# Performance work log

Measured on AMD Instinct MI355X. Metric: run time of the kernel, lower is better.

## Reference

```python
import jax, jax.numpy as jnp
import numpy as np

EMBED_DIM = 2048
NUM_HEADS = 32
NUM_SEQS = 8
SEQ_LEN = 1024
TOTAL_TOKENS = NUM_SEQS * SEQ_LEN


def setup_inputs() -> dict:
    key = jax.random.key(0)
    ks = jax.random.split(key, 9)
    E = EMBED_DIM
    std = 0.02
    return {
        "hidden_states": jax.random.normal(ks[0], (TOTAL_TOKENS, E), dtype=jnp.float32),
        "Wq": jax.random.normal(ks[1], (E, E), dtype=jnp.float32) * std,
        "bq": jax.random.normal(ks[2], (E,), dtype=jnp.float32) * std,
        "Wk": jax.random.normal(ks[3], (E, E), dtype=jnp.float32) * std,
        "bk": jax.random.normal(ks[4], (E,), dtype=jnp.float32) * std,
        "Wv": jax.random.normal(ks[5], (E, E), dtype=jnp.float32) * std,
        "bv": jax.random.normal(ks[6], (E,), dtype=jnp.float32) * std,
        "Wo": jax.random.normal(ks[7], (E, E), dtype=jnp.float32) * std,
        "bo": jax.random.normal(ks[8], (E,), dtype=jnp.float32) * std,
        "seq_len": SEQ_LEN,
    }


def reference(hidden_states, Wq, bq, Wk, bk, Wv, bv, Wo, bo, seq_len):
    # OPTAttention (has_cache=False): block-diagonal causal attention over
    # packed ragged sequences; here all NUM_SEQS sequences have length seq_len,
    # so the block-diagonal mask is exactly per-sequence causal attention.
    T, E = hidden_states.shape
    H = NUM_HEADS
    D = E // H
    B = T // seq_len
    scaling = D ** -0.5

    # torch nn.Linear: y = x @ W.T + b
    q = hidden_states @ Wq.T + bq
    k = hidden_states @ Wk.T + bk
    v = hidden_states @ Wv.T + bv

    q = q.reshape(B, seq_len, H, D)
    k = k.reshape(B, seq_len, H, D)
    v = v.reshape(B, seq_len, H, D)

    # [B, H, S, S] attention scores (xformers applies scale to q@k.T)
    scores = jnp.einsum("bqhd,bkhd->bhqk", q, k) * scaling
    causal = jnp.tril(jnp.ones((seq_len, seq_len), dtype=bool))
    scores = jnp.where(causal[None, None, :, :], scores, jnp.finfo(scores.dtype).min)
    probs = jax.nn.softmax(scores, axis=-1)

    attn = jnp.einsum("bhqk,bkhd->bqhd", probs, v)  # [B, S, H, D]
    attn = attn.reshape(T, E)
    return attn @ Wo.T + bo
```

## Files before the change

kernel.cpp:

```cpp
#include <hip/hip_runtime.h>
#include <hip/hip_bf16.h>

typedef __bf16 bf16_t;
typedef __bf16 bf16x8 __attribute__((ext_vector_type(8)));
typedef __bf16 bf16x4 __attribute__((ext_vector_type(4)));
typedef float f32x4 __attribute__((ext_vector_type(4)));
typedef float f32x16 __attribute__((ext_vector_type(16)));
typedef unsigned short u16x8 __attribute__((ext_vector_type(8)));
typedef unsigned int u32x4 __attribute__((ext_vector_type(4)));

#define T_TOK 8192
#define E_DIM 2048
#define NHEAD 32
#define SEQLEN 1024
#define NSEQ 8
#define LDQ 6144

#if __has_builtin(__builtin_amdgcn_exp2f)
#define EXP2F(x) __builtin_amdgcn_exp2f(x)
#else
#define EXP2F(x) exp2f(x)
#endif

static __device__ inline unsigned cvtpk_bf16(float lo, float hi) {
    unsigned r;
    asm("v_cvt_pk_bf16_f32 %0, %1, %2" : "=v"(r) : "v"(lo), "v"(hi));
    return r;
}

static __device__ inline void plswap(unsigned &x, unsigned &y, bool lo_half) {
#if __has_builtin(__builtin_amdgcn_permlane32_swap)
    auto r = __builtin_amdgcn_permlane32_swap(x, y, false, false);
    x = r[0]; y = r[1];
#else
    unsigned xs = __shfl_xor(x, 32), ys = __shfl_xor(y, 32);
    unsigned nx = lo_half ? x : ys;
    unsigned ny = lo_half ? xs : y;
    x = nx; y = ny;
#endif
}

__global__ void cvt_f32_bf16(const float* __restrict__ in, bf16_t* __restrict__ out, int n4) {
    int idx = blockIdx.x * blockDim.x + threadIdx.x;
    int stride = gridDim.x * blockDim.x;
    for (int i = idx; i < n4; i += stride) {
        const float4 v = reinterpret_cast<const float4*>(in)[i];
        bf16x4 o;
        o[0] = (bf16_t)v.x; o[1] = (bf16_t)v.y; o[2] = (bf16_t)v.z; o[3] = (bf16_t)v.w;
        reinterpret_cast<bf16x4*>(out)[i] = o;
    }
}

template<bool OUT_BF16>
__global__ __launch_bounds__(512, 2)
void gemm256r(const bf16_t* __restrict__ A, const bf16_t* __restrict__ B,
              const float* __restrict__ b0, const float* __restrict__ b1,
              const float* __restrict__ b2, void* __restrict__ Cout,
              int M, int N, float qs, int qlim) {
    constexpr int K = 2048;
    constexpr int NK = K / 32;
    __shared__ alignas(16) unsigned char lds[131072];
    const int tid = threadIdx.x;
    const int wid = tid >> 6, l = tid & 63;
    const int cpx = gridDim.x >> 3;
    const int wg = (blockIdx.x & 7) * cpx + (blockIdx.x >> 3);
    const int nbm = M >> 8;
    const int bm = wg % nbm, bn = wg / nbm;
    const int wrow = (wid >> 2) * 128, wcol = (wid & 3) * 64;
    const int lr = l & 15, lg = l >> 4;

    f32x4 acc[8][4] = {};

    const bf16_t* aBase = A + (size_t)(bm * 256) * K;
    const bf16_t* bBase = B + (size_t)(bn * 256) * K;
    const int sr = l >> 2;
    const int sc = (l & 3) * 16;

    auto stage = [&](int t) {
        unsigned char* base = lds + (t & 3) * 32768;
#pragma unroll
        for (int c = 0; c < 2; ++c) {
            const int chunk = wid * 2 + c;
            const int r = chunk * 16 + sr;
            const int cb = sc ^ (((r >> 1) & 3) << 4);
            __builtin_amdgcn_global_load_lds(
                (const __attribute__((address_space(1))) void*)(aBase + (size_t)r * K + t * 32 + (cb >> 1)),
                (__attribute__((address_space(3))) void*)(base + chunk * 1024), 16, 0, 0);
            __builtin_amdgcn_global_load_lds(
                (const __attribute__((address_space(1))) void*)(bBase + (size_t)r * K + t * 32 + (cb >> 1)),
                (__attribute__((address_space(3))) void*)(base + 16384 + chunk * 1024), 16, 0, 0);
        }
    };

    stage(0); stage(1); stage(2);
    asm volatile("s_waitcnt vmcnt(8)" ::: "memory");
    __builtin_amdgcn_s_barrier();

    for (int t = 0; t < NK; ++t) {
        if (t + 3 < NK) stage(t + 3);
        const unsigned char* Ab = lds + (t & 3) * 32768;
        const unsigned char* Bb = Ab + 16384;
        bf16x8 bfv[4], af[8];
#pragma unroll
        for (int n = 0; n < 4; ++n) {
            const int r = wcol + n * 16 + lr;
            bfv[n] = *reinterpret_cast<const bf16x8*>(Bb + r * 64 + ((lg * 16) ^ (((r >> 1) & 3) << 4)));
        }
#pragma unroll
        for (int m = 0; m < 8; ++m) {
            const int r = wrow + m * 16 + lr;
            af[m] = *reinterpret_cast<const bf16x8*>(Ab + r * 64 + ((lg * 16) ^ (((r >> 1) & 3) << 4)));
        }
        __builtin_amdgcn_s_setprio(1);
#pragma unroll
        for (int m = 0; m < 8; ++m)
#pragma unroll
            for (int n = 0; n < 4; ++n)
                acc[m][n] = __builtin_amdgcn_mfma_f32_16x16x32_bf16(af[m], bfv[n], acc[m][n], 0, 0, 0);
        __builtin_amdgcn_s_setprio(0);
        if (t == NK - 1) break;
        if (t + 3 < NK)      asm volatile("s_waitcnt vmcnt(8)" ::: "memory");
        else if (t + 2 < NK) asm volatile("s_waitcnt vmcnt(4)" ::: "memory");
        else                 asm volatile("s_waitcnt vmcnt(0)" ::: "memory");
        __builtin_amdgcn_s_barrier();
    }

    const int r0 = bm * 256 + wrow + lg * 4;
    const int c0 = bn * 256 + wcol + lr;
#pragma unroll
    for (int n = 0; n < 4; ++n) {
        const int cc = c0 + n * 16;
        const float bias = (cc < 2048) ? b0[cc] : (cc < 4096 ? b1[cc - 2048] : b2[cc - 4096]);
        const float sc2 = (cc < qlim) ? qs : 1.0f;
#pragma unroll
        for (int m = 0; m < 8; ++m)
#pragma unroll
            for (int j = 0; j < 4; ++j) {
                const int rr = r0 + m * 16 + j;
                const float v = (acc[m][n][j] + bias) * sc2;
                if (OUT_BF16) ((bf16_t*)Cout)[(size_t)rr * N + cc] = (bf16_t)v;
                else          ((float*)Cout)[(size_t)rr * N + cc] = v;
            }
    }
}

__global__ __launch_bounds__(512, 2)
void attn_fwd3(const bf16_t* __restrict__ QKV, bf16_t* __restrict__ Og) {
    const int orig = blockIdx.x;
    const int id = (orig & 7) * 64 + (orig >> 3);
    const int grp = id >> 1;
    const int pairIdx = id & 1;
    const int h = grp & 31;
    const int sq = grp >> 5;

    const int tid = threadIdx.x;
    const int w = tid >> 6;
    const int l = tid & 63;
    const int ll = l & 31;
    const int hi = l >> 5;
    const bool lo_half = (hi == 0);

    __shared__ alignas(16) unsigned char lds[65536];

    const bf16_t* Qg = QKV;
    const bf16_t* Kg = QKV + 2048;
    const bf16_t* Vg = QKV + 4096;
    const size_t kvbase = (size_t)(sq * SEQLEN) * LDQ + h * 64;

    bf16x8 vr0, vr1;
    const int vk0 = l * 2;
    const int vd0 = w * 8;

    auto stageK = [&](int kt, int buf) {
#pragma unroll
        for (int c = 0; c < 2; ++c) {
            const int o = (w * 2 + c) * 1024 + l * 16;
            const int r = o >> 7;
            const int swb = (o & 127) ^ ((r & 7) << 4);
            const bf16_t* src = Kg + kvbase + (size_t)(kt * 128 + r) * LDQ + (swb >> 1);
            __builtin_amdgcn_global_load_lds(
                (const __attribute__((address_space(1))) void*)src,
                (__attribute__((address_space(3))) void*)(lds + buf * 16384 + (w * 2 + c) * 1024),
                16, 0, 0);
        }
    };
    auto loadV = [&](int kt) {
        const bf16_t* vp = Vg + kvbase + (size_t)(kt * 128 + vk0) * LDQ + vd0;
        vr0 = *reinterpret_cast<const bf16x8*>(vp);
        vr1 = *reinterpret_cast<const bf16x8*>(vp + LDQ);
    };
    auto writeV = [&](int buf) {
        u16x8 s0 = __builtin_bit_cast(u16x8, vr0);
        u16x8 s1 = __builtin_bit_cast(u16x8, vr1);
        unsigned char* vb = lds + 32768 + buf * 16384;
#pragma unroll
        for (int e = 0; e < 8; ++e) {
            const int d = vd0 + e;
            unsigned off = (unsigned)(d * 256 + vk0 * 2);
            off ^= ((unsigned)((d ^ (d >> 4)) & 15)) << 4;
            *reinterpret_cast<unsigned*>(vb + off) = (unsigned)s0[e] | ((unsigned)s1[e] << 16);
        }
    };

    const unsigned ksw = (unsigned)((l & 7) << 4);
    const unsigned kbase = (unsigned)(ll * 128 + hi * 16);

#pragma unroll 1
    for (int seg = 0; seg < 2; ++seg) {
        const int qt = pairIdx ? (seg ? 2 : 1) : (seg ? 3 : 0);

        const int q_glob = qt * 256 + w * 32 + ll;
        const bf16_t* qp = Qg + (size_t)(sq * SEQLEN + q_glob) * LDQ + h * 64 + hi * 8;
        bf16x8 qf[4];
#pragma unroll
        for (int dc = 0; dc < 4; ++dc)
            qf[dc] = *reinterpret_cast<const bf16x8*>(qp + dc * 16);

        const int nkt = 2 * qt + 2;
        const int q_wave_max = qt * 256 + w * 32 + 31;

        f32x16 oac[2] = {};
        float mrun = -3.0e38f, lsum = 0.f;

        stageK(0, 0);
        loadV(0);
        writeV(0);
        __syncthreads();

        int cur = 0;
        for (int kt = 0; kt < nkt; ++kt) {
            const bool notlast = (kt + 1 < nkt);
            if (notlast) { stageK(kt + 1, cur ^ 1); loadV(kt + 1); }

            if (kt * 128 <= q_wave_max) {
                const unsigned char* Kcur = lds + cur * 16384;
                const unsigned char* Vcur = lds + 32768 + cur * 16384;

                f32x16 st[4];
#pragma unroll
                for (int kh = 0; kh < 4; ++kh) {
                    f32x16 acc = {};
#pragma unroll
                    for (int dc = 0; dc < 4; ++dc) {
                        const unsigned off = (kbase + (unsigned)(kh * 4096 + dc * 32)) ^ ksw;
                        const bf16x8 ka = *reinterpret_cast<const bf16x8*>(Kcur + off);
                        acc = __builtin_amdgcn_mfma_f32_32x32x16_bf16(ka, qf[dc], acc, 0, 0, 0);
                    }
                    st[kh] = acc;
                }

                if (kt >= 2 * qt) {
#pragma unroll
                    for (int kh = 0; kh < 4; ++kh)
#pragma unroll
                        for (int r = 0; r < 16; ++r) {
                            const int kg = kt * 128 + kh * 32 + (r & 3) + 8 * (r >> 2) + 4 * hi;
                            if (kg > q_glob) st[kh][r] = -3.0e38f;
                        }
                }

                float tm = -3.0e38f;
#pragma unroll
                for (int kh = 0; kh < 4; ++kh)
#pragma unroll
                    for (int r = 0; r < 16; ++r) tm = fmaxf(tm, st[kh][r]);
                tm = fmaxf(tm, __shfl_xor(tm, 32));

                if (!__all(tm <= mrun + 8.0f)) {
                    const float mnew = fmaxf(mrun, tm);
                    const float rsc = EXP2F(mrun - mnew);
                    mrun = mnew;
                    lsum *= rsc;
#pragma unroll
                    for (int dh = 0; dh < 2; ++dh)
#pragma unroll
                        for (int r = 0; r < 16; ++r) oac[dh][r] *= rsc;
                }

                float ps = 0.f;
#pragma unroll
                for (int kh = 0; kh < 4; ++kh)
#pragma unroll
                    for (int r = 0; r < 16; ++r) {
                        const float p = EXP2F(st[kh][r] - mrun);
                        st[kh][r] = p;
                        ps += p;
                    }
                ps += __shfl_xor(ps, 32);
                lsum += ps;

                bf16x8 pf[8];
#pragma unroll
                for (int kh = 0; kh < 4; ++kh)
#pragma unroll
                    for (int hc = 0; hc < 2; ++hc) {
                        const int b0i = hc * 8;
                        unsigned a  = cvtpk_bf16(st[kh][b0i + 0], st[kh][b0i + 1]);
                        unsigned b  = cvtpk_bf16(st[kh][b0i + 4], st[kh][b0i + 5]);
                        unsigned a2 = cvtpk_bf16(st[kh][b0i + 2], st[kh][b0i + 3]);
                        unsigned b2 = cvtpk_bf16(st[kh][b0i + 6], st[kh][b0i + 7]);
                        plswap(a, b, lo_half);
                        plswap(a2, b2, lo_half);
                        u32x4 words = { a, a2, b, b2 };
                        pf[kh * 2 + hc] = __builtin_bit_cast(bf16x8, words);
                    }

#pragma unroll
                for (int dh = 0; dh < 2; ++dh) {
                    const int d = dh * 32 + ll;
                    const unsigned vsw = ((unsigned)((d ^ (d >> 4)) & 15)) << 4;
                    const unsigned vbb = (unsigned)(d * 256 + hi * 16);
#pragma unroll
                    for (int kc = 0; kc < 8; ++kc) {
                        const unsigned off = (vbb + (unsigned)(kc * 32)) ^ vsw;
                        const bf16x8 vfr = *reinterpret_cast<const bf16x8*>(Vcur + off);
                        oac[dh] = __builtin_amdgcn_mfma_f32_32x32x16_bf16(vfr, pf[kc], oac[dh], 0, 0, 0);
                    }
                }
            }

            if (notlast) writeV(cur ^ 1);
            __syncthreads();
            cur ^= 1;
        }

        const float inv = 1.0f / lsum;
        bf16_t* op = Og + (size_t)(sq * SEQLEN + q_glob) * E_DIM + h * 64;
#pragma unroll
        for (int dh = 0; dh < 2; ++dh)
#pragma unroll
            for (int rq = 0; rq < 4; ++rq) {
                const int d0 = dh * 32 + 8 * rq + 4 * hi;
                bf16x4 ov;
#pragma unroll
                for (int j = 0; j < 4; ++j)
                    ov[j] = (bf16_t)(oac[dh][rq * 4 + j] * inv);
                *reinterpret_cast<bf16x4*>(op + d0) = ov;
            }
    }
}

extern "C" void kernel_launch(void* const* d_in, const int* in_sizes, int n_in,
                              void* d_out, int out_size, void* d_ws, size_t ws_size,
                              hipStream_t stream) {
    const float* hid = (const float*)d_in[0];
    const float* Wq  = (const float*)d_in[1];
    const float* bq  = (const float*)d_in[2];
    const float* Wk  = (const float*)d_in[3];
    const float* bk  = (const float*)d_in[4];
    const float* Wv  = (const float*)d_in[5];
    const float* bv  = (const float*)d_in[6];
    const float* Wo  = (const float*)d_in[7];
    const float* bo  = (const float*)d_in[8];
    float* out = (float*)d_out;

    const size_t TE = (size_t)T_TOK * E_DIM;
    const size_t EE = (size_t)E_DIM * E_DIM;

    bf16_t* ws   = (bf16_t*)d_ws;
    bf16_t* hidB = ws;
    bf16_t* qkvB = ws + TE;
    bf16_t* Wcat = qkvB + 3 * TE;
    bf16_t* WoB  = Wcat + 3 * EE;

    cvt_f32_bf16<<<2048, 256, 0, stream>>>(hid, hidB, (int)(TE / 4));
    cvt_f32_bf16<<<1024, 256, 0, stream>>>(Wq, Wcat, (int)(EE / 4));
    cvt_f32_bf16<<<1024, 256, 0, stream>>>(Wk, Wcat + EE, (int)(EE / 4));
    cvt_f32_bf16<<<1024, 256, 0, stream>>>(Wv, Wcat + 2 * EE, (int)(EE / 4));
    cvt_f32_bf16<<<1024, 256, 0, stream>>>(Wo, WoB, (int)(EE / 4));

    const float QSCALE = 0.125f * 1.4426950408889634f;

    gemm256r<true><<<dim3((T_TOK / 256) * (LDQ / 256)), 512, 0, stream>>>(
        hidB, Wcat, bq, bk, bv, qkvB, T_TOK, LDQ, QSCALE, 2048);

    attn_fwd3<<<dim3(512), 512, 0, stream>>>(qkvB, hidB);

    gemm256r<false><<<dim3((T_TOK / 256) * (E_DIM / 256)), 512, 0, stream>>>(
        hidB, WoB, bo, bo, bo, out, T_TOK, E_DIM, 1.0f, 0);
}
```

Baseline: 410.4 us.

## Double-buffer GEMM register fragments and merge conversion kernels into one launch

The GEMM main loop now loads the next K-step's A/B fragments from LDS into a second register set while MFMAs run on the current set. This hides LDS read latency behind matrix math, and the prefetch depth is adjusted to match. The five fp32-to-bf16 conversion launches are merged into a single kernel that picks its source by block index, which cuts launch overhead. The extra fragment registers raise register pressure, which could hurt occupancy at 2 waves per SIMD.

```diff
diff --git a/kernel.cpp b/kernel.cpp
--- a/kernel.cpp
+++ b/kernel.cpp
@@ -40,20 +40,33 @@
 #endif
 }
 
-__global__ void cvt_f32_bf16(const float* __restrict__ in, bf16_t* __restrict__ out, int n4) {
-    int idx = blockIdx.x * blockDim.x + threadIdx.x;
-    int stride = gridDim.x * blockDim.x;
-    for (int i = idx; i < n4; i += stride) {
-        const float4 v = reinterpret_cast<const float4*>(in)[i];
+__global__ void cvt_all(const float* __restrict__ hid, const float* __restrict__ Wq,
+                        const float* __restrict__ Wk, const float* __restrict__ Wv,
+                        const float* __restrict__ Wo, bf16_t* __restrict__ hidB,
+                        bf16_t* __restrict__ Wcat, bf16_t* __restrict__ WoB) {
+    const int TE4 = (T_TOK * E_DIM) / 4;
+    const int EE4 = (E_DIM * E_DIM) / 4;
+    const float* src;
+    bf16_t* dst;
+    int n4, base, nb;
+    const int bid = blockIdx.x;
+    if (bid < 2048)      { src = hid; dst = hidB;              n4 = TE4; base = 0;    nb = 2048; }
+    else if (bid < 2560) { src = Wq;  dst = Wcat;              n4 = EE4; base = 2048; nb = 512; }
+    else if (bid < 3072) { src = Wk;  dst = Wcat + 4 * EE4;    n4 = EE4; base = 2560; nb = 512; }
+    else if (bid < 3584) { src = Wv;  dst = Wcat + 8 * EE4;    n4 = EE4; base = 3072; nb = 512; }
+    else                 { src = Wo;  dst = WoB;               n4 = EE4; base = 3584; nb = 512; }
+    const int stride = nb * 256;
+    for (int i = (bid - base) * 256 + threadIdx.x; i < n4; i += stride) {
+        const float4 v = reinterpret_cast<const float4*>(src)[i];
         bf16x4 o;
         o[0] = (bf16_t)v.x; o[1] = (bf16_t)v.y; o[2] = (bf16_t)v.z; o[3] = (bf16_t)v.w;
-        reinterpret_cast<bf16x4*>(out)[i] = o;
+        reinterpret_cast<bf16x4*>(dst)[i] = o;
     }
 }
 
 template<bool OUT_BF16>
 __global__ __launch_bounds__(512, 2)
-void gemm256r(const bf16_t* __restrict__ A, const bf16_t* __restrict__ B,
+void gemm256f(const bf16_t* __restrict__ A, const bf16_t* __restrict__ B,
               const float* __restrict__ b0, const float* __restrict__ b1,
               const float* __restrict__ b2, void* __restrict__ Cout,
               int M, int N, float qs, int qlim) {
@@ -92,37 +105,56 @@
         }
     };
 
+    bf16x8 fa0[8], fb0[4], fa1[8], fb1[4];
+
     stage(0); stage(1); stage(2);
-    asm volatile("s_waitcnt vmcnt(8)" ::: "memory");
+    asm volatile("s_waitcnt vmcnt(4)" ::: "memory");
     __builtin_amdgcn_s_barrier();
-
-    for (int t = 0; t < NK; ++t) {
-        if (t + 3 < NK) stage(t + 3);
-        const unsigned char* Ab = lds + (t & 3) * 32768;
+    {
+        const unsigned char* Ab = lds;
         const unsigned char* Bb = Ab + 16384;
-        bf16x8 bfv[4], af[8];
 #pragma unroll
         for (int n = 0; n < 4; ++n) {
             const int r = wcol + n * 16 + lr;
-            bfv[n] = *reinterpret_cast<const bf16x8*>(Bb + r * 64 + ((lg * 16) ^ (((r >> 1) & 3) << 4)));
+            fb0[n] = *reinterpret_cast<const bf16x8*>(Bb + r * 64 + ((lg * 16) ^ (((r >> 1) & 3) << 4)));
         }
 #pragma unroll
         for (int m = 0; m < 8; ++m) {
             const int r = wrow + m * 16 + lr;
-            af[m] = *reinterpret_cast<const bf16x8*>(Ab + r * 64 + ((lg * 16) ^ (((r >> 1) & 3) << 4)));
-        }
+            fa0[m] = *reinterpret_cast<const bf16x8*>(Ab + r * 64 + ((lg * 16) ^ (((r >> 1) & 3) << 4)));
+        }
+    }
+
+    auto step = [&](int t, bf16x8 (&ca)[8], bf16x8 (&cb)[4],
+                    bf16x8 (&na)[8], bf16x8 (&nb)[4]) {
+        if (t + 3 < NK) stage(t + 3);
+        const unsigned char* Nb = lds + ((t + 1) & 3) * 32768;
+        const unsigned char* NbB = Nb + 16384;
         __builtin_amdgcn_s_setprio(1);
 #pragma unroll
-        for (int m = 0; m < 8; ++m)
+        for (int m = 0; m < 8; ++m) {
+            if (m < 4) {
+                const int rb = wcol + m * 16 + lr;
+                nb[m] = *reinterpret_cast<const bf16x8*>(NbB + rb * 64 + ((lg * 16) ^ (((rb >> 1) & 3) << 4)));
+            }
+            const int ra = wrow + m * 16 + lr;
+            na[m] = *reinterpret_cast<const bf16x8*>(Nb + ra * 64 + ((lg * 16) ^ (((ra >> 1) & 3) << 4)));
 #pragma unroll
             for (int n = 0; n < 4; ++n)
-                acc[m][n] = __builtin_amdgcn_mfma_f32_16x16x32_bf16(af[m], bfv[n], acc[m][n], 0, 0, 0);
+                acc[m][n] = __builtin_amdgcn_mfma_f32_16x16x32_bf16(ca[m], cb[n], acc[m][n], 0, 0, 0);
+        }
         __builtin_amdgcn_s_setprio(0);
-        if (t == NK - 1) break;
-        if (t + 3 < NK)      asm volatile("s_waitcnt vmcnt(8)" ::: "memory");
-        else if (t + 2 < NK) asm volatile("s_waitcnt vmcnt(4)" ::: "memory");
-        else                 asm volatile("s_waitcnt vmcnt(0)" ::: "memory");
-        __builtin_amdgcn_s_barrier();
+        if (t < NK - 1) {
+            if (t + 3 < NK) asm volatile("s_waitcnt vmcnt(4)" ::: "memory");
+            else            asm volatile("s_waitcnt vmcnt(0)" ::: "memory");
+            __builtin_amdgcn_s_barrier();
+        }
+    };
+
+#pragma unroll 1
+    for (int t = 0; t < NK; t += 2) {
+        step(t,     fa0, fb0, fa1, fb1);
+        step(t + 1, fa1, fb1, fa0, fb0);
     }
 
     const int r0 = bm * 256 + wrow + lg * 4;
@@ -363,19 +395,15 @@
     bf16_t* Wcat = qkvB + 3 * TE;
     bf16_t* WoB  = Wcat + 3 * EE;
 
-    cvt_f32_bf16<<<2048, 256, 0, stream>>>(hid, hidB, (int)(TE / 4));
-    cvt_f32_bf16<<<1024, 256, 0, stream>>>(Wq, Wcat, (int)(EE / 4));
-    cvt_f32_bf16<<<1024, 256, 0, stream>>>(Wk, Wcat + EE, (int)(EE / 4));
-    cvt_f32_bf16<<<1024, 256, 0, stream>>>(Wv, Wcat + 2 * EE, (int)(EE / 4));
-    cvt_f32_bf16<<<1024, 256, 0, stream>>>(Wo, WoB, (int)(EE / 4));
+    cvt_all<<<4096, 256, 0, stream>>>(hid, Wq, Wk, Wv, Wo, hidB, Wcat, WoB);
 
     const float QSCALE = 0.125f * 1.4426950408889634f;
 
-    gemm256r<true><<<dim3((T_TOK / 256) * (LDQ / 256)), 512, 0, stream>>>(
+    gemm256f<true><<<dim3((T_TOK / 256) * (LDQ / 256)), 512, 0, stream>>>(
         hidB, Wcat, bq, bk, bv, qkvB, T_TOK, LDQ, QSCALE, 2048);
 
     attn_fwd3<<<dim3(512), 512, 0, stream>>>(qkvB, hidB);
 
-    gemm256r<false><<<dim3((T_TOK / 256) * (E_DIM / 256)), 512, 0, stream>>>(
+    gemm256f<false><<<dim3((T_TOK / 256) * (E_DIM / 256)), 512, 0, stream>>>(
         hidB, WoB, bo, bo, bo, out, T_TOK, E_DIM, 1.0f, 0);
 }
```

Result: faster. 397.9 us (-3.0%).
